# Performance work log

Measured on AMD Instinct MI355X. Metric: run time of the kernel, lower is better.

## Reference

```python
import math
import jax, jax.numpy as jnp
import numpy as np

D_MODEL = 768
N_HEADS = 12
HEAD_DIM = D_MODEL // N_HEADS
D_FF = 3072
LN_EPS = 1e-5


def _alibi_slopes(n_heads):
    def pow2(n):
        start = 2 ** (-(2 ** (-(math.log2(n) - 3))))
        return [start * start ** i for i in range(n)]
    if n_heads & (n_heads - 1) == 0:
        s = pow2(n_heads)
    else:
        c = 2 ** math.floor(math.log2(n_heads))
        s = pow2(c) + pow2(2 * c)[0::2][: n_heads - c]
    return np.asarray(s, dtype=np.float32)  # positive; negated at use site


def _ln(t, g, b):
    m = jnp.mean(t, axis=-1, keepdims=True)
    v = jnp.mean(jnp.square(t - m), axis=-1, keepdims=True)
    return (t - m) * jax.lax.rsqrt(v + LN_EPS) * g + b


def setup_inputs() -> dict:
    key = jax.random.key(0)
    ks = jax.random.split(key, 12)
    B, N = 4, 1025
    s = 0.02
    inp = {
        "x": jax.random.normal(ks[0], (B, N, D_MODEL), dtype=jnp.float32),
        "positions": jax.random.normal(ks[1], (B, N, 2), dtype=jnp.float32) * 8.0,
        "patch_sizes": jax.random.uniform(ks[2], (B,), dtype=jnp.float32, minval=0.5, maxval=2.0),
        "num_registers": 0,
        "ln1_g": jnp.ones((D_MODEL,), jnp.float32),
        "ln1_b": jnp.zeros((D_MODEL,), jnp.float32),
        "wq": jax.random.normal(ks[3], (D_MODEL, D_MODEL), jnp.float32) * s,
        "bq": jnp.zeros((D_MODEL,), jnp.float32),
        "wk": jax.random.normal(ks[4], (D_MODEL, D_MODEL), jnp.float32) * s,
        "bk": jnp.zeros((D_MODEL,), jnp.float32),
        "wv": jax.random.normal(ks[5], (D_MODEL, D_MODEL), jnp.float32) * s,
        "bv": jnp.zeros((D_MODEL,), jnp.float32),
        "wo": jax.random.normal(ks[6], (D_MODEL, D_MODEL), jnp.float32) * s,
        "bo": jnp.zeros((D_MODEL,), jnp.float32),
        "qn_g": jnp.ones((HEAD_DIM,), jnp.float32),
        "qn_b": jnp.zeros((HEAD_DIM,), jnp.float32),
        "kn_g": jnp.ones((HEAD_DIM,), jnp.float32),
        "kn_b": jnp.zeros((HEAD_DIM,), jnp.float32),
        "ln2_g": jnp.ones((D_MODEL,), jnp.float32),
        "ln2_b": jnp.zeros((D_MODEL,), jnp.float32),
        "w1": jax.random.normal(ks[7], (D_MODEL, D_FF), jnp.float32) * s,
        "b1": jnp.zeros((D_FF,), jnp.float32),
        "w2": jax.random.normal(ks[8], (D_FF, D_MODEL), jnp.float32) * s,
        "b2": jnp.zeros((D_MODEL,), jnp.float32),
    }
    return inp


def reference(x, positions, patch_sizes, num_registers,
              ln1_g, ln1_b, wq, bq, wk, bk, wv, bv, wo, bo,
              qn_g, qn_b, kn_g, kn_b, ln2_g, ln2_b, w1, b1, w2, b2):
    B, N, d = x.shape
    H, HD = N_HEADS, HEAD_DIM

    xn = _ln(x, ln1_g, ln1_b)
    q = (xn @ wq + bq).reshape(B, N, H, HD).transpose(0, 2, 1, 3)  # [B,H,N,HD]
    k = (xn @ wk + bk).reshape(B, N, H, HD).transpose(0, 2, 1, 3)
    v = (xn @ wv + bv).reshape(B, N, H, HD).transpose(0, 2, 1, 3)
    q = _ln(q, qn_g, qn_b)  # qk-norm over head_dim
    k = _ln(k, kn_g, kn_b)

    # 2-D ALiBi bias: [B,H,N,N]
    slopes = jnp.asarray(_alibi_slopes(H))  # positive
    ps = jnp.clip(patch_sizes, 1e-6)[:, None, None]
    diff = positions[:, :, None, :] - positions[:, None, :, :]  # [B,N,N,2]
    dist = jnp.sqrt(jnp.sum(jnp.square(diff), axis=-1)) / ps  # [B,N,N]
    bias = -slopes[None, :, None, None] * dist[:, None, :, :]
    idx = jnp.arange(N)
    special = (idx == 0) | ((idx >= 1) & (idx < 1 + num_registers))  # CLS + registers
    keep = (~special).astype(x.dtype)
    bias = bias * keep[None, None, :, None] * keep[None, None, None, :]

    scale = 1.0 / math.sqrt(HD)
    scores = jnp.einsum('bhqd,bhkd->bhqk', q, k) * scale + bias
    attn = jax.nn.softmax(scores, axis=-1)
    o = jnp.einsum('bhqk,bhkd->bhqd', attn, v)
    o = o.transpose(0, 2, 1, 3).reshape(B, N, d) @ wo + bo
    x = x + o

    xn2 = _ln(x, ln2_g, ln2_b)
    mlp = jax.nn.gelu(xn2 @ w1 + b1, approximate=False) @ w2 + b2
    return x + mlp
```

## Files before the change

### kernel.cpp

```cpp
#include <hip/hip_runtime.h>
#include <hip/hip_bf16.h>
#include <math.h>

typedef __attribute__((ext_vector_type(4))) float f32x4;
typedef __attribute__((ext_vector_type(8))) short short8;

#define DMODEL 768
#define NH 12
#define HD 64
#define DFF 3072
#define KVB 64
#define NSPLIT 2
#define QH 2
#define NP 1040

__device__ __forceinline__ short f2bf(float f) {
    union { float f; unsigned int u; } c; c.f = f;
    unsigned int r = c.u + 0x7FFFu + ((c.u >> 16) & 1u);
    return (short)(r >> 16);
}

__device__ __forceinline__ float bf2f(short s) {
    union { unsigned int u; float f; } c; c.u = ((unsigned int)(unsigned short)s) << 16;
    return c.f;
}

__device__ __forceinline__ void gload16(const void* g, void* l) {
    __builtin_amdgcn_global_load_lds((const __attribute__((address_space(1))) void*)g,
                                     (__attribute__((address_space(3))) void*)l, 16, 0, 0);
}

__device__ __forceinline__ int xcd_swz(int o, int nwg) {
    int q = nwg >> 3, r = nwg & 7, x = o & 7, i = o >> 3;
    return (x < r ? x * (q + 1) : r * (q + 1) + (x - r) * q) + i;
}

__global__ __launch_bounds__(256) void transpose_cast(const float* __restrict__ src,
                                                      short* __restrict__ dst, int K, int Nn) {
    __shared__ float tile[32][33];
    const int n0 = blockIdx.x * 32, k0 = blockIdx.y * 32;
    const int tx = threadIdx.x & 31, ty = threadIdx.x >> 5;
    #pragma unroll
    for (int i = ty; i < 32; i += 8) {
        int k = k0 + i, n = n0 + tx;
        tile[i][tx] = (k < K && n < Nn) ? src[(size_t)k * Nn + n] : 0.f;
    }
    __syncthreads();
    #pragma unroll
    for (int i = ty; i < 32; i += 8) {
        int n = n0 + i, k = k0 + tx;
        if (n < Nn && k < K) dst[(size_t)n * K + k] = f2bf(tile[tx][i]);
    }
}

__global__ void concat_bias(const float* __restrict__ bq, const float* __restrict__ bk,
                            const float* __restrict__ bv, float* __restrict__ out) {
    int i = blockIdx.x * 256 + threadIdx.x;
    if (i < 2304) out[i] = (i < 768) ? bq[i] : (i < 1536 ? bk[i - 768] : bv[i - 1536]);
}

__global__ __launch_bounds__(256) void ln_rows(const float* __restrict__ x, const float* __restrict__ g,
                                               const float* __restrict__ bb, short* __restrict__ out, int M) {
    __shared__ float red[8];
    const int row = blockIdx.x;
    const int tid = threadIdx.x;
    const float* xr = x + (size_t)row * DMODEL;
    float v[3];
    #pragma unroll
    for (int j = 0; j < 3; j++) v[j] = xr[tid + j * 256];
    float s = v[0] + v[1] + v[2];
    #pragma unroll
    for (int mk = 32; mk; mk >>= 1) s += __shfl_xor(s, mk);
    if ((tid & 63) == 0) red[tid >> 6] = s;
    __syncthreads();
    const float mean = (red[0] + red[1] + red[2] + red[3]) * (1.0f / 768.0f);
    float sq = 0.f;
    #pragma unroll
    for (int j = 0; j < 3; j++) { float d = v[j] - mean; sq += d * d; }
    #pragma unroll
    for (int mk = 32; mk; mk >>= 1) sq += __shfl_xor(sq, mk);
    if ((tid & 63) == 0) red[4 + (tid >> 6)] = sq;
    __syncthreads();
    const float var = (red[4] + red[5] + red[6] + red[7]) * (1.0f / 768.0f);
    const float rstd = rsqrtf(var + 1e-5f);
    short* orow = out + (size_t)row * DMODEL;
    #pragma unroll
    for (int j = 0; j < 3; j++) {
        int col = tid + j * 256;
        orow[col] = f2bf((v[j] - mean) * rstd * g[col] + bb[col]);
    }
}

__global__ __launch_bounds__(256) void gemm_qkv(const short* __restrict__ A, const short* __restrict__ Bt,
        const float* __restrict__ bias,
        const float* __restrict__ qg, const float* __restrict__ qb2,
        const float* __restrict__ kg, const float* __restrict__ kb2,
        short* __restrict__ Qb, short* __restrict__ Kb, short* __restrict__ Vtp,
        int M, int B, int Nseq) {
    __shared__ short As[64 * 64];
    __shared__ short Bs[128 * 64];
    const int nbx = 18, nby = (M + 63) / 64;
    const int sid = xcd_swz(blockIdx.x, nbx * nby);
    const int n0 = (sid % nbx) * 128, m0 = (sid / nbx) * 64;
    const int tid = threadIdx.x, w = tid >> 6, lane = tid & 63, g = lane >> 4, cl = lane & 15;
    const int wm = w >> 1, wn = w & 1;
    f32x4 acc[2][4];
    #pragma unroll
    for (int a = 0; a < 2; a++)
        #pragma unroll
        for (int b2 = 0; b2 < 4; b2++) acc[a][b2] = (f32x4){0.f, 0.f, 0.f, 0.f};
    for (int kk = 0; kk < 768; kk += 64) {
        #pragma unroll
        for (int c = 0; c < 1536; c += 256) {
            int ci = c + tid;
            if (ci < 512) {
                int row = ci >> 3, p = ci & 7;
                int arow = m0 + row; if (arow >= M) arow = M - 1;
                gload16(A + (size_t)arow * 768 + kk + ((p ^ (row & 7)) << 3), &As[ci * 8]);
            } else {
                int c2 = ci - 512;
                int row = c2 >> 3, p = c2 & 7;
                gload16(Bt + (size_t)(n0 + row) * 768 + kk + ((p ^ (row & 7)) << 3), &Bs[c2 * 8]);
            }
        }
        __syncthreads();
        #pragma unroll
        for (int kh = 0; kh < 2; ++kh) {
            short8 af[2], bf[4];
            #pragma unroll
            for (int mi = 0; mi < 2; mi++) {
                int ra = wm * 32 + mi * 16 + cl;
                af[mi] = *(const short8*)&As[ra * 64 + ((((kh << 2) + g) ^ (ra & 7)) << 3)];
            }
            #pragma unroll
            for (int ni = 0; ni < 4; ni++) {
                int rb = wn * 64 + ni * 16 + cl;
                bf[ni] = *(const short8*)&Bs[rb * 64 + ((((kh << 2) + g) ^ (rb & 7)) << 3)];
            }
            #pragma unroll
            for (int mi = 0; mi < 2; mi++)
                #pragma unroll
                for (int ni = 0; ni < 4; ni++)
                    acc[mi][ni] = __builtin_amdgcn_mfma_f32_16x16x32_bf16(af[mi], bf[ni], acc[mi][ni], 0, 0, 0);
        }
        __syncthreads();
    }
    const int t = n0 / 768;
    const int h = (n0 - t * 768) / 64 + wn;
    const int b0 = m0 / Nseq, bnd = (b0 + 1) * Nseq;
    float bi[4];
    #pragma unroll
    for (int ni = 0; ni < 4; ni++) bi[ni] = bias[n0 + wn * 64 + ni * 16 + cl];
    if (t < 2) {
        const float* gp = (t == 0) ? qg : kg;
        const float* bp = (t == 0) ? qb2 : kb2;
        float gv[4], bv[4];
        #pragma unroll
        for (int ni = 0; ni < 4; ni++) { gv[ni] = gp[ni * 16 + cl]; bv[ni] = bp[ni * 16 + cl]; }
        short* out = (t == 0) ? Qb : Kb;
        #pragma unroll
        for (int mi = 0; mi < 2; mi++)
            #pragma unroll
            for (int r = 0; r < 4; r++) {
                int row = m0 + wm * 32 + mi * 16 + 4 * g + r;
                float v0 = acc[mi][0][r] + bi[0];
                float v1 = acc[mi][1][r] + bi[1];
                float v2 = acc[mi][2][r] + bi[2];
                float v3 = acc[mi][3][r] + bi[3];
                float sx = v0 + v1 + v2 + v3;
                float sxx = v0 * v0 + v1 * v1 + v2 * v2 + v3 * v3;
                #pragma unroll
                for (int mk = 8; mk; mk >>= 1) { sx += __shfl_xor(sx, mk); sxx += __shfl_xor(sxx, mk); }
                float mean = sx * (1.0f / 64.0f);
                float var = sxx * (1.0f / 64.0f) - mean * mean;
                float rstd = rsqrtf(var + 1e-5f);
                if (row < M) {
                    int bb = (row >= bnd) ? b0 + 1 : b0;
                    int n = row - bb * Nseq;
                    size_t base = (((size_t)bb * NH + h) * Nseq + n) * HD + cl;
                    out[base + 0]  = f2bf(fmaf((v0 - mean) * rstd, gv[0], bv[0]));
                    out[base + 16] = f2bf(fmaf((v1 - mean) * rstd, gv[1], bv[1]));
                    out[base + 32] = f2bf(fmaf((v2 - mean) * rstd, gv[2], bv[2]));
                    out[base + 48] = f2bf(fmaf((v3 - mean) * rstd, gv[3], bv[3]));
                }
            }
    } else {
        #pragma unroll
        for (int mi = 0; mi < 2; mi++)
            #pragma unroll
            for (int r = 0; r < 4; r++) {
                int row = m0 + wm * 32 + mi * 16 + 4 * g + r;
                if (row < M) {
                    int bb = (row >= bnd) ? b0 + 1 : b0;
                    int n = row - bb * Nseq;
                    size_t vb2 = ((size_t)bb * NH + h) * HD + cl;
                    #pragma unroll
                    for (int ni = 0; ni < 4; ni++)
                        Vtp[(vb2 + ni * 16) * NP + n] = f2bf(acc[mi][ni][r] + bi[ni]);
                }
            }
    }
}

template<int EPI, int BM, int BN>
__global__ __launch_bounds__(256) void gemm_bt(const short* __restrict__ A, const short* __restrict__ Bt,
        const float* __restrict__ bias, const float* __restrict__ res, void* __restrict__ Cv,
        int M, int Nn, int K) {
    constexpr int RN = BN / 32;
    __shared__ short As[BM * 64];
    __shared__ short Bs[BN * 64];
    const int nbx = Nn / BN, nby = (M + BM - 1) / BM;
    const int sid = xcd_swz(blockIdx.x, nbx * nby);
    const int n0 = (sid % nbx) * BN, m0 = (sid / nbx) * BM;
    const int tid = threadIdx.x, w = tid >> 6, lane = tid & 63, g = lane >> 4, cl = lane & 15;
    const int wm = w >> 1, wn = w & 1;
    f32x4 acc[2][RN];
    #pragma unroll
    for (int a = 0; a < 2; a++)
        #pragma unroll
        for (int b2 = 0; b2 < RN; b2++) acc[a][b2] = (f32x4){0.f, 0.f, 0.f, 0.f};
    constexpr int CHA = BM * 8, CHT = (BM + BN) * 8;
    for (int kk = 0; kk < K; kk += 64) {
        #pragma unroll
        for (int c = 0; c < CHT; c += 256) {
            int ci = c + tid;
            if (ci < CHA) {
                int row = ci >> 3, p = ci & 7;
                int arow = m0 + row; if (arow >= M) arow = M - 1;
                gload16(A + (size_t)arow * K + kk + ((p ^ (row & 7)) << 3), &As[ci * 8]);
            } else {
                int c2 = ci - CHA;
                int row = c2 >> 3, p = c2 & 7;
                gload16(Bt + (size_t)(n0 + row) * K + kk + ((p ^ (row & 7)) << 3), &Bs[c2 * 8]);
            }
        }
        __syncthreads();
        #pragma unroll
        for (int kh = 0; kh < 2; ++kh) {
            short8 af[2], bf[RN];
            #pragma unroll
            for (int mi = 0; mi < 2; mi++) {
                int ra = wm * (BM / 2) + mi * 16 + cl;
                af[mi] = *(const short8*)&As[ra * 64 + ((((kh << 2) + g) ^ (ra & 7)) << 3)];
            }
            #pragma unroll
            for (int ni = 0; ni < RN; ni++) {
                int rb = wn * (BN / 2) + ni * 16 + cl;
                bf[ni] = *(const short8*)&Bs[rb * 64 + ((((kh << 2) + g) ^ (rb & 7)) << 3)];
            }
            #pragma unroll
            for (int mi = 0; mi < 2; mi++)
                #pragma unroll
                for (int ni = 0; ni < RN; ni++)
                    acc[mi][ni] = __builtin_amdgcn_mfma_f32_16x16x32_bf16(af[mi], bf[ni], acc[mi][ni], 0, 0, 0);
        }
        __syncthreads();
    }
    #pragma unroll
    for (int ni = 0; ni < RN; ++ni) {
        int col = n0 + wn * (BN / 2) + ni * 16 + cl;
        float bi = bias[col];
        #pragma unroll
        for (int mi = 0; mi < 2; ++mi) {
            int rb = m0 + wm * (BM / 2) + mi * 16 + 4 * g;
            #pragma unroll
            for (int r = 0; r < 4; ++r) {
                int row = rb + r;
                if (row < M) {
                    float vv = acc[mi][ni][r] + bi;
                    if (EPI == 1) {
                        vv += res[(size_t)row * Nn + col];
                        ((float*)Cv)[(size_t)row * Nn + col] = vv;
                    } else {
                        float ge = 0.5f * vv * (1.0f + erff(vv * 0.70710678118654752f));
                        ((short*)Cv)[(size_t)row * Nn + col] = f2bf(ge);
                    }
                }
            }
        }
    }
}

__global__ __launch_bounds__(256, 2) void attn_kernel(
        const short* __restrict__ Qb, const short* __restrict__ Kb, const short* __restrict__ Vt,
        const float* __restrict__ pos, const float* __restrict__ psz, const int* __restrict__ nregp,
        short* __restrict__ opart, float* __restrict__ ppart, int B, int Nn, int nwg) {
    __shared__ short Vbuf[2][QH][4096];
    __shared__ short Pl[4][QH][16][68];
    const int nqt = (Nn + 63) >> 6;
    const int sid = xcd_swz(blockIdx.x, nwg);
    const int qt = sid % nqt;
    const int rem = sid / nqt;
    const int nyy = (NH / QH) * NSPLIT;
    const int yy = rem % nyy;
    const int b = rem / nyy;
    const int h0 = (yy / NSPLIT) * QH, sp = yy % NSPLIT;
    const int tid = threadIdx.x, w = tid >> 6, lane = tid & 63, g = lane >> 4, cl = lane & 15;
    const int nreg1 = 1 + nregp[0];
    const float inv_ps = 1.0f / fmaxf(psz[b], 1e-6f);
    const float sc2 = 0.125f * 1.4426950408889634f;
    const size_t bq = (size_t)b * Nn;
    const float2* __restrict__ pos2 = (const float2*)pos;
    const int q0 = qt * 64 + w * 16;

    size_t bh[QH], vb[QH];
    float slopeP[QH];
    short8 qa[QH][2];
    int qr = q0 + cl; if (qr > Nn - 1) qr = Nn - 1;
    #pragma unroll
    for (int hh = 0; hh < QH; hh++) {
        int h = h0 + hh;
        bh[hh] = ((size_t)b * NH + h) * (size_t)Nn;
        vb[hh] = ((size_t)b * NH + h) * (size_t)(HD * NP);
        float slope = (h < 8) ? exp2f(-(float)(h + 1)) : exp2f(-0.5f - (float)(h - 8));
        slopeP[hh] = slope * inv_ps * 1.4426950408889634f;
        const short* qptr = Qb + (bh[hh] + qr) * HD;
        qa[hh][0] = *(const short8*)(qptr + 8 * g);
        qa[hh][1] = *(const short8*)(qptr + 32 + 8 * g);
    }

    int qi[4]; float qpx[4], qpy[4], sP[QH][4];
    #pragma unroll
    for (int i = 0; i < 4; i++) {
        qi[i] = q0 + 4 * g + i;
        int qc = qi[i] < Nn ? qi[i] : Nn - 1;
        float2 qp = pos2[bq + qc];
        qpx[i] = qp.x; qpy[i] = qp.y;
        float keepq = (qc < nreg1) ? 0.f : 1.f;
        #pragma unroll
        for (int hh = 0; hh < QH; hh++) sP[hh][i] = slopeP[hh] * keepq;
    }

    f32x4 o[QH][4];
    float psum[QH][4];
    #pragma unroll
    for (int hh = 0; hh < QH; hh++)
        #pragma unroll
        for (int c2 = 0; c2 < 4; c2++) { o[hh][c2] = (f32x4){0.f, 0.f, 0.f, 0.f}; psum[hh][c2] = 0.f; }

    const int ktiles = (Nn + KVB - 1) / KVB;
    const int ktfull = Nn / KVB;
    const int tps = (ktiles + NSPLIT - 1) / NSPLIT;
    const int t0 = sp * tps, t1 = min(ktiles, t0 + tps);

    auto stage = [&](int buf, int kt) {
        const int kv0 = kt * KVB;
        #pragma unroll
        for (int it = 0; it < 2 * QH; ++it) {
            int idx = it * 256 + tid;
            int hh = idx >> 9, rm = idx & 511;
            int d = rm >> 3, slot = rm & 7;
            int kvs = kv0 + ((slot ^ (d & 7)) << 3);
            gload16(Vt + vb[hh] + (size_t)d * NP + kvs, &Vbuf[buf][hh][rm * 8]);
        }
    };

    stage(0, t0);
    int cur = 0;
    for (int kt = t0; kt < t1; ++kt) {
        const int kv0 = kt * KVB;
        __syncthreads();
        if (kt + 1 < t1) stage(cur ^ 1, kt + 1);

        if (kt < ktfull) {
            #pragma unroll
            for (int half = 0; half < 4; ++half) {
                const int kc = kv0 + half * 16 + cl;
                const short* kp0 = Kb + (bh[0] + kc) * HD;
                const short* kp1 = Kb + (bh[1] + kc) * HD;
                const short8 ka0 = *(const short8*)(kp0 + 8 * g);
                const short8 ka1 = *(const short8*)(kp0 + 32 + 8 * g);
                const short8 kb0 = *(const short8*)(kp1 + 8 * g);
                const short8 kb1 = *(const short8*)(kp1 + 32 + 8 * g);
                f32x4 s0 = __builtin_amdgcn_mfma_f32_16x16x32_bf16(qa[0][0], ka0, (f32x4){0.f,0.f,0.f,0.f}, 0, 0, 0);
                s0 = __builtin_amdgcn_mfma_f32_16x16x32_bf16(qa[0][1], ka1, s0, 0, 0, 0);
                f32x4 s1 = __builtin_amdgcn_mfma_f32_16x16x32_bf16(qa[1][0], kb0, (f32x4){0.f,0.f,0.f,0.f}, 0, 0, 0);
                s1 = __builtin_amdgcn_mfma_f32_16x16x32_bf16(qa[1][1], kb1, s1, 0, 0, 0);
                const float2 kp2 = pos2[bq + kc];
                const float kpk = (kc < nreg1) ? 0.f : 1.f;
                #pragma unroll
                for (int i = 0; i < 4; i++) {
                    float dx = qpx[i] - kp2.x, dy = qpy[i] - kp2.y;
                    float dist = sqrtf(fmaf(dx, dx, dy * dy)) * kpk;
                    float e0 = fmaf(s0[i], sc2, -12.0f);
                    e0 = fmaf(-sP[0][i], dist, e0);
                    float p0 = exp2f(e0);
                    unsigned int pu0 = __float_as_uint(p0) & 0xffff0000u;
                    psum[0][i] += __uint_as_float(pu0);
                    Pl[w][0][4 * g + i][half * 16 + cl] = (short)(pu0 >> 16);
                    float e1 = fmaf(s1[i], sc2, -12.0f);
                    e1 = fmaf(-sP[1][i], dist, e1);
                    float p1 = exp2f(e1);
                    unsigned int pu1 = __float_as_uint(p1) & 0xffff0000u;
                    psum[1][i] += __uint_as_float(pu1);
                    Pl[w][1][4 * g + i][half * 16 + cl] = (short)(pu1 >> 16);
                }
            }
        } else {
            #pragma unroll
            for (int half = 0; half < 4; ++half) {
                const int kc = kv0 + half * 16 + cl;
                const int kcc = kc < Nn ? kc : Nn - 1;
                const short* kp0 = Kb + (bh[0] + kcc) * HD;
                const short* kp1 = Kb + (bh[1] + kcc) * HD;
                const short8 ka0 = *(const short8*)(kp0 + 8 * g);
                const short8 ka1 = *(const short8*)(kp0 + 32 + 8 * g);
                const short8 kb0 = *(const short8*)(kp1 + 8 * g);
                const short8 kb1 = *(const short8*)(kp1 + 32 + 8 * g);
                f32x4 s0 = __builtin_amdgcn_mfma_f32_16x16x32_bf16(qa[0][0], ka0, (f32x4){0.f,0.f,0.f,0.f}, 0, 0, 0);
                s0 = __builtin_amdgcn_mfma_f32_16x16x32_bf16(qa[0][1], ka1, s0, 0, 0, 0);
                f32x4 s1 = __builtin_amdgcn_mfma_f32_16x16x32_bf16(qa[1][0], kb0, (f32x4){0.f,0.f,0.f,0.f}, 0, 0, 0);
                s1 = __builtin_amdgcn_mfma_f32_16x16x32_bf16(qa[1][1], kb1, s1, 0, 0, 0);
                const float2 kp2 = pos2[bq + kcc];
                const float kpk = (kcc < nreg1) ? 0.f : 1.f;
                const bool valid = kc < Nn;
                #pragma unroll
                for (int i = 0; i < 4; i++) {
                    float dx = qpx[i] - kp2.x, dy = qpy[i] - kp2.y;
                    float dist = sqrtf(fmaf(dx, dx, dy * dy)) * kpk;
                    float e0 = fmaf(s0[i], sc2, -12.0f);
                    e0 = fmaf(-sP[0][i], dist, e0);
                    float p0 = valid ? exp2f(e0) : 0.f;
                    unsigned int pu0 = __float_as_uint(p0) & 0xffff0000u;
                    psum[0][i] += __uint_as_float(pu0);
                    Pl[w][0][4 * g + i][half * 16 + cl] = (short)(pu0 >> 16);
                    float e1 = fmaf(s1[i], sc2, -12.0f);
                    e1 = fmaf(-sP[1][i], dist, e1);
                    float p1 = valid ? exp2f(e1) : 0.f;
                    unsigned int pu1 = __float_as_uint(p1) & 0xffff0000u;
                    psum[1][i] += __uint_as_float(pu1);
                    Pl[w][1][4 * g + i][half * 16 + cl] = (short)(pu1 >> 16);
                }
            }
        }
        #pragma unroll
        for (int hh = 0; hh < QH; hh++) {
            #pragma unroll
            for (int ks = 0; ks < 2; ++ks) {
                const short8 pf = *(const short8*)&Pl[w][hh][cl][ks * 32 + 8 * g];
                #pragma unroll
                for (int c2 = 0; c2 < 4; c2++) {
                    const int d = c2 * 16 + cl;
                    const int slot = ((ks << 2) + g) ^ (cl & 7);
                    const short8 vf = *(const short8*)&Vbuf[cur][hh][d * 64 + slot * 8];
                    o[hh][c2] = __builtin_amdgcn_mfma_f32_16x16x32_bf16(pf, vf, o[hh][c2], 0, 0, 0);
                }
            }
        }
        cur ^= 1;
    }
    #pragma unroll
    for (int i = 0; i < 4; i++) {
        float rs[QH];
        #pragma unroll
        for (int hh = 0; hh < QH; hh++) {
            rs[hh] = psum[hh][i];
            #pragma unroll
            for (int mk = 8; mk; mk >>= 1) rs[hh] += __shfl_xor(rs[hh], mk);
        }
        if (qi[i] < Nn) {
            #pragma unroll
            for (int hh = 0; hh < QH; hh++) {
                size_t rbase = (((size_t)sp * B + b) * NH + (h0 + hh)) * Nn + qi[i];
                #pragma unroll
                for (int c2 = 0; c2 < 4; c2++)
                    opart[rbase * HD + c2 * 16 + cl] = f2bf(o[hh][c2][i]);
                if (cl == 0) ppart[rbase] = rs[hh];
            }
        }
    }
}

__global__ __launch_bounds__(256) void attn_reduce(const short* __restrict__ opart,
        const float* __restrict__ ppart, short* __restrict__ Ob, int B, int Nn) {
    const int rows = B * NH * Nn;
    const int row = blockIdx.x * 4 + (threadIdx.x >> 6);
    if (row >= rows) return;
    const int d = threadIdx.x & 63;
    const int n = row % Nn;
    const int bh = row / Nn;
    const int h = bh % NH, b = bh / NH;
    const size_t stride = (size_t)B * NH * Nn;
    float o = 0.f, p = 0.f;
    #pragma unroll
    for (int s = 0; s < NSPLIT; s++) {
        o += bf2f(opart[((size_t)s * stride + row) * HD + d]);
        p += ppart[(size_t)s * stride + row];
    }
    Ob[((size_t)b * Nn + n) * DMODEL + h * HD + d] = f2bf(o / p);
}

extern "C" void kernel_launch(void* const* d_in, const int* in_sizes, int n_in,
                              void* d_out, int out_size, void* d_ws, size_t ws_size,
                              hipStream_t stream) {
    const float* x    = (const float*)d_in[0];
    const float* pos  = (const float*)d_in[1];
    const float* psz  = (const float*)d_in[2];
    const int*   nreg = (const int*)d_in[3];
    const float* ln1g = (const float*)d_in[4];
    const float* ln1b = (const float*)d_in[5];
    const float* wq   = (const float*)d_in[6];
    const float* bq   = (const float*)d_in[7];
    const float* wk   = (const float*)d_in[8];
    const float* bk   = (const float*)d_in[9];
    const float* wv   = (const float*)d_in[10];
    const float* bv   = (const float*)d_in[11];
    const float* wo   = (const float*)d_in[12];
    const float* bo   = (const float*)d_in[13];
    const float* qng  = (const float*)d_in[14];
    const float* qnb  = (const float*)d_in[15];
    const float* kng  = (const float*)d_in[16];
    const float* knb  = (const float*)d_in[17];
    const float* ln2g = (const float*)d_in[18];
    const float* ln2b = (const float*)d_in[19];
    const float* w1   = (const float*)d_in[20];
    const float* b1   = (const float*)d_in[21];
    const float* w2   = (const float*)d_in[22];
    const float* b2   = (const float*)d_in[23];

    const int B  = in_sizes[2];
    const int Nn = in_sizes[1] / (2 * B);
    const int M  = B * Nn;

    char* ws = (char*)d_ws;
    size_t off = 0;
    auto alloc = [&](size_t bytes) -> char* {
        char* p = ws + off;
        off += (bytes + 255) & ~(size_t)255;
        return p;
    };
    short* wt_qkv   = (short*)alloc((size_t)2304 * 768 * 2);
    short* wt_o     = (short*)alloc((size_t)768 * 768 * 2);
    short* wt_1     = (short*)alloc((size_t)3072 * 768 * 2);
    short* wt_2     = (short*)alloc((size_t)768 * 3072 * 2);
    float* bias_qkv = (float*)alloc(2304 * 4);
    short* xn       = (short*)alloc((size_t)M * 768 * 2);
    short* Qb       = (short*)alloc((size_t)M * 768 * 2);
    short* Kb       = (short*)alloc((size_t)M * 768 * 2);
    short* Vt       = (short*)alloc((size_t)B * NH * HD * NP * 2 + 4096);
    short* Ob       = (short*)alloc((size_t)M * 768 * 2);
    float* x1       = (float*)alloc((size_t)M * 768 * 4);
    short* xn2      = (short*)alloc((size_t)M * 768 * 2);
    short* hmid     = (short*)alloc((size_t)M * 3072 * 2);
    float* ppart    = (float*)alloc((size_t)NSPLIT * B * NH * Nn * 4);
    short* opart    = hmid;

    dim3 blk(256);
    transpose_cast<<<dim3(24, 24), blk, 0, stream>>>(wq, wt_qkv, 768, 768);
    transpose_cast<<<dim3(24, 24), blk, 0, stream>>>(wk, wt_qkv + 768 * 768, 768, 768);
    transpose_cast<<<dim3(24, 24), blk, 0, stream>>>(wv, wt_qkv + 2 * 768 * 768, 768, 768);
    transpose_cast<<<dim3(24, 24), blk, 0, stream>>>(wo, wt_o, 768, 768);
    transpose_cast<<<dim3(96, 24), blk, 0, stream>>>(w1, wt_1, 768, 3072);
    transpose_cast<<<dim3(24, 96), blk, 0, stream>>>(w2, wt_2, 3072, 768);
    concat_bias<<<9, blk, 0, stream>>>(bq, bk, bv, bias_qkv);

    const int MB64 = (M + 63) / 64;
    ln_rows<<<M, blk, 0, stream>>>(x, ln1g, ln1b, xn, M);
    gemm_qkv<<<18 * MB64, blk, 0, stream>>>(xn, wt_qkv, bias_qkv, qng, qnb, kng, knb,
                                            Qb, Kb, Vt, M, B, Nn);
    const int nqt = (Nn + 63) / 64;
    const int anwg = nqt * (NH / QH) * NSPLIT * B;
    attn_kernel<<<anwg, blk, 0, stream>>>(Qb, Kb, Vt, pos, psz, nreg, opart, ppart, B, Nn, anwg);
    attn_reduce<<<(B * NH * Nn + 3) / 4, blk, 0, stream>>>(opart, ppart, Ob, B, Nn);
    gemm_bt<1, 64, 64><<<12 * MB64, blk, 0, stream>>>(Ob, wt_o, bo, x, x1, M, 768, 768);
    ln_rows<<<M, blk, 0, stream>>>(x1, ln2g, ln2b, xn2, M);
    gemm_bt<2, 64, 128><<<24 * MB64, blk, 0, stream>>>(xn2, wt_1, b1, nullptr, hmid, M, 3072, 768);
    gemm_bt<1, 64, 64><<<12 * MB64, blk, 0, stream>>>(hmid, wt_2, b2, x1, (float*)d_out, M, 768, 3072);
}
```

Baseline: 270.1 us.

## Transpose QK MFMA so each lane owns one query, pack P to bf16, split KV three ways

Swaps the MFMA operand order so each lane holds scores for a single query row across four keys. Per-query position, slope and keep factors then collapse to scalars, and per-iteration mask work is only specialised in for tiles touching the CLS/register tokens. P values are converted with packed bf16 conversion and written as 32-bit words into a padded LDS tile. Row sums are reduced with fewer shuffles plus an LDS exchange. KV is split three ways with launch bounds raised to three blocks per CU, which may raise register pressure and adds partial-result reduction work. The row sums now accumulate unrounded fp32 p rather than the bf16-truncated values used in PV.

```diff
diff --git a/kernel.cpp b/kernel.cpp
--- a/kernel.cpp
+++ b/kernel.cpp
@@ -10,9 +10,12 @@
 #define HD 64
 #define DFF 3072
 #define KVB 64
-#define NSPLIT 2
+#define NSPLIT 3
 #define QH 2
 #define NP 1040
+
+struct FalseC { static constexpr bool v = false; };
+struct TrueC  { static constexpr bool v = true;  };
 
 __device__ __forceinline__ short f2bf(float f) {
     union { float f; unsigned int u; } c; c.f = f;
@@ -281,12 +284,13 @@
     }
 }
 
-__global__ __launch_bounds__(256, 2) void attn_kernel(
+__global__ __launch_bounds__(256, 3) void attn_kernel(
         const short* __restrict__ Qb, const short* __restrict__ Kb, const short* __restrict__ Vt,
         const float* __restrict__ pos, const float* __restrict__ psz, const int* __restrict__ nregp,
         short* __restrict__ opart, float* __restrict__ ppart, int B, int Nn, int nwg) {
     __shared__ short Vbuf[2][QH][4096];
-    __shared__ short Pl[4][QH][16][68];
+    __shared__ short Pl[4][QH][16][72];
+    __shared__ float Rs[4][QH][16];
     const int nqt = (Nn + 63) >> 6;
     const int sid = xcd_swz(blockIdx.x, nwg);
     const int qt = sid % nqt;
@@ -304,42 +308,35 @@
     const int q0 = qt * 64 + w * 16;
 
     size_t bh[QH], vb[QH];
-    float slopeP[QH];
     short8 qa[QH][2];
+    float sP[QH];
     int qr = q0 + cl; if (qr > Nn - 1) qr = Nn - 1;
+    const float2 qp = pos2[bq + qr];
+    const float keepq = (qr < nreg1) ? 0.f : 1.f;
     #pragma unroll
     for (int hh = 0; hh < QH; hh++) {
         int h = h0 + hh;
         bh[hh] = ((size_t)b * NH + h) * (size_t)Nn;
         vb[hh] = ((size_t)b * NH + h) * (size_t)(HD * NP);
         float slope = (h < 8) ? exp2f(-(float)(h + 1)) : exp2f(-0.5f - (float)(h - 8));
-        slopeP[hh] = slope * inv_ps * 1.4426950408889634f;
+        sP[hh] = slope * inv_ps * 1.4426950408889634f * keepq;
         const short* qptr = Qb + (bh[hh] + qr) * HD;
         qa[hh][0] = *(const short8*)(qptr + 8 * g);
         qa[hh][1] = *(const short8*)(qptr + 32 + 8 * g);
     }
 
-    int qi[4]; float qpx[4], qpy[4], sP[QH][4];
-    #pragma unroll
-    for (int i = 0; i < 4; i++) {
-        qi[i] = q0 + 4 * g + i;
-        int qc = qi[i] < Nn ? qi[i] : Nn - 1;
-        float2 qp = pos2[bq + qc];
-        qpx[i] = qp.x; qpy[i] = qp.y;
-        float keepq = (qc < nreg1) ? 0.f : 1.f;
-        #pragma unroll
-        for (int hh = 0; hh < QH; hh++) sP[hh][i] = slopeP[hh] * keepq;
-    }
+    int qi[4];
+    #pragma unroll
+    for (int i = 0; i < 4; i++) qi[i] = q0 + 4 * g + i;
 
     f32x4 o[QH][4];
-    float psum[QH][4];
+    float psum[QH] = {0.f, 0.f};
     #pragma unroll
     for (int hh = 0; hh < QH; hh++)
         #pragma unroll
-        for (int c2 = 0; c2 < 4; c2++) { o[hh][c2] = (f32x4){0.f, 0.f, 0.f, 0.f}; psum[hh][c2] = 0.f; }
+        for (int c2 = 0; c2 < 4; c2++) o[hh][c2] = (f32x4){0.f, 0.f, 0.f, 0.f};
 
     const int ktiles = (Nn + KVB - 1) / KVB;
-    const int ktfull = Nn / KVB;
     const int tps = (ktiles + NSPLIT - 1) / NSPLIT;
     const int t0 = sp * tps, t1 = min(ktiles, t0 + tps);
 
@@ -362,77 +359,67 @@
         __syncthreads();
         if (kt + 1 < t1) stage(cur ^ 1, kt + 1);
 
-        if (kt < ktfull) {
-            #pragma unroll
-            for (int half = 0; half < 4; ++half) {
-                const int kc = kv0 + half * 16 + cl;
-                const short* kp0 = Kb + (bh[0] + kc) * HD;
-                const short* kp1 = Kb + (bh[1] + kc) * HD;
-                const short8 ka0 = *(const short8*)(kp0 + 8 * g);
-                const short8 ka1 = *(const short8*)(kp0 + 32 + 8 * g);
-                const short8 kb0 = *(const short8*)(kp1 + 8 * g);
-                const short8 kb1 = *(const short8*)(kp1 + 32 + 8 * g);
-                f32x4 s0 = __builtin_amdgcn_mfma_f32_16x16x32_bf16(qa[0][0], ka0, (f32x4){0.f,0.f,0.f,0.f}, 0, 0, 0);
-                s0 = __builtin_amdgcn_mfma_f32_16x16x32_bf16(qa[0][1], ka1, s0, 0, 0, 0);
-                f32x4 s1 = __builtin_amdgcn_mfma_f32_16x16x32_bf16(qa[1][0], kb0, (f32x4){0.f,0.f,0.f,0.f}, 0, 0, 0);
-                s1 = __builtin_amdgcn_mfma_f32_16x16x32_bf16(qa[1][1], kb1, s1, 0, 0, 0);
-                const float2 kp2 = pos2[bq + kc];
-                const float kpk = (kc < nreg1) ? 0.f : 1.f;
-                #pragma unroll
-                for (int i = 0; i < 4; i++) {
-                    float dx = qpx[i] - kp2.x, dy = qpy[i] - kp2.y;
-                    float dist = sqrtf(fmaf(dx, dx, dy * dy)) * kpk;
-                    float e0 = fmaf(s0[i], sc2, -12.0f);
-                    e0 = fmaf(-sP[0][i], dist, e0);
-                    float p0 = exp2f(e0);
-                    unsigned int pu0 = __float_as_uint(p0) & 0xffff0000u;
-                    psum[0][i] += __uint_as_float(pu0);
-                    Pl[w][0][4 * g + i][half * 16 + cl] = (short)(pu0 >> 16);
-                    float e1 = fmaf(s1[i], sc2, -12.0f);
-                    e1 = fmaf(-sP[1][i], dist, e1);
-                    float p1 = exp2f(e1);
-                    unsigned int pu1 = __float_as_uint(p1) & 0xffff0000u;
-                    psum[1][i] += __uint_as_float(pu1);
-                    Pl[w][1][4 * g + i][half * 16 + cl] = (short)(pu1 >> 16);
-                }
+        auto qbody = [&](int qt2, auto mc, auto tc) {
+            constexpr bool KMASK = decltype(mc)::v;
+            constexpr bool TAIL  = decltype(tc)::v;
+            const int kbase = kv0 + qt2 * 16;
+            int krow = kbase + cl;
+            if (TAIL) krow = min(krow, Nn - 1);
+            const short* kp0 = Kb + (bh[0] + krow) * HD;
+            const short* kp1 = Kb + (bh[1] + krow) * HD;
+            const short8 k00 = *(const short8*)(kp0 + 8 * g);
+            const short8 k01 = *(const short8*)(kp0 + 32 + 8 * g);
+            const short8 k10 = *(const short8*)(kp1 + 8 * g);
+            const short8 k11 = *(const short8*)(kp1 + 32 + 8 * g);
+            f32x4 s0 = __builtin_amdgcn_mfma_f32_16x16x32_bf16(k00, qa[0][0], (f32x4){0.f,0.f,0.f,0.f}, 0, 0, 0);
+            s0 = __builtin_amdgcn_mfma_f32_16x16x32_bf16(k01, qa[0][1], s0, 0, 0, 0);
+            f32x4 s1 = __builtin_amdgcn_mfma_f32_16x16x32_bf16(k10, qa[1][0], (f32x4){0.f,0.f,0.f,0.f}, 0, 0, 0);
+            s1 = __builtin_amdgcn_mfma_f32_16x16x32_bf16(k11, qa[1][1], s1, 0, 0, 0);
+            const int kb4 = kbase + 4 * g;
+            float p0v[4], p1v[4];
+            #pragma unroll
+            for (int i = 0; i < 4; i++) {
+                int ki = kb4 + i;
+                int kic = TAIL ? min(ki, Nn - 1) : ki;
+                float2 kp2 = pos2[bq + kic];
+                float dx = qp.x - kp2.x, dy = qp.y - kp2.y;
+                float dist = sqrtf(fmaf(dx, dx, dy * dy));
+                if (KMASK) dist *= (ki < nreg1) ? 0.f : 1.f;
+                float e0 = fmaf(s0[i], sc2, -12.0f);
+                e0 = fmaf(-sP[0], dist, e0);
+                float p0 = exp2f(e0);
+                float e1 = fmaf(s1[i], sc2, -12.0f);
+                e1 = fmaf(-sP[1], dist, e1);
+                float p1 = exp2f(e1);
+                if (TAIL) { bool vl = ki < Nn; p0 = vl ? p0 : 0.f; p1 = vl ? p1 : 0.f; }
+                psum[0] += p0; psum[1] += p1;
+                p0v[i] = p0; p1v[i] = p1;
+            }
+            unsigned int w00, w01, w10, w11;
+            asm("v_cvt_pk_bf16_f32 %0, %1, %2" : "=v"(w00) : "v"(p0v[0]), "v"(p0v[1]));
+            asm("v_cvt_pk_bf16_f32 %0, %1, %2" : "=v"(w01) : "v"(p0v[2]), "v"(p0v[3]));
+            asm("v_cvt_pk_bf16_f32 %0, %1, %2" : "=v"(w10) : "v"(p1v[0]), "v"(p1v[1]));
+            asm("v_cvt_pk_bf16_f32 %0, %1, %2" : "=v"(w11) : "v"(p1v[2]), "v"(p1v[3]));
+            *(unsigned int*)&Pl[w][0][cl][qt2 * 16 + 4 * g]     = w00;
+            *(unsigned int*)&Pl[w][0][cl][qt2 * 16 + 4 * g + 2] = w01;
+            *(unsigned int*)&Pl[w][1][cl][qt2 * 16 + 4 * g]     = w10;
+            *(unsigned int*)&Pl[w][1][cl][qt2 * 16 + 4 * g + 2] = w11;
+        };
+
+        const bool istail = (kv0 + KVB > Nn);
+        if (!istail) {
+            if (kv0 < nreg1) {
+                qbody(0, TrueC{}, FalseC{}); qbody(1, TrueC{}, FalseC{});
+                qbody(2, TrueC{}, FalseC{}); qbody(3, TrueC{}, FalseC{});
+            } else {
+                qbody(0, FalseC{}, FalseC{}); qbody(1, FalseC{}, FalseC{});
+                qbody(2, FalseC{}, FalseC{}); qbody(3, FalseC{}, FalseC{});
             }
         } else {
-            #pragma unroll
-            for (int half = 0; half < 4; ++half) {
-                const int kc = kv0 + half * 16 + cl;
-                const int kcc = kc < Nn ? kc : Nn - 1;
-                const short* kp0 = Kb + (bh[0] + kcc) * HD;
-                const short* kp1 = Kb + (bh[1] + kcc) * HD;
-                const short8 ka0 = *(const short8*)(kp0 + 8 * g);
-                const short8 ka1 = *(const short8*)(kp0 + 32 + 8 * g);
-                const short8 kb0 = *(const short8*)(kp1 + 8 * g);
-                const short8 kb1 = *(const short8*)(kp1 + 32 + 8 * g);
-                f32x4 s0 = __builtin_amdgcn_mfma_f32_16x16x32_bf16(qa[0][0], ka0, (f32x4){0.f,0.f,0.f,0.f}, 0, 0, 0);
-                s0 = __builtin_amdgcn_mfma_f32_16x16x32_bf16(qa[0][1], ka1, s0, 0, 0, 0);
-                f32x4 s1 = __builtin_amdgcn_mfma_f32_16x16x32_bf16(qa[1][0], kb0, (f32x4){0.f,0.f,0.f,0.f}, 0, 0, 0);
-                s1 = __builtin_amdgcn_mfma_f32_16x16x32_bf16(qa[1][1], kb1, s1, 0, 0, 0);
-                const float2 kp2 = pos2[bq + kcc];
-                const float kpk = (kcc < nreg1) ? 0.f : 1.f;
-                const bool valid = kc < Nn;
-                #pragma unroll
-                for (int i = 0; i < 4; i++) {
-                    float dx = qpx[i] - kp2.x, dy = qpy[i] - kp2.y;
-                    float dist = sqrtf(fmaf(dx, dx, dy * dy)) * kpk;
-                    float e0 = fmaf(s0[i], sc2, -12.0f);
-                    e0 = fmaf(-sP[0][i], dist, e0);
-                    float p0 = valid ? exp2f(e0) : 0.f;
-                    unsigned int pu0 = __float_as_uint(p0) & 0xffff0000u;
-                    psum[0][i] += __uint_as_float(pu0);
-                    Pl[w][0][4 * g + i][half * 16 + cl] = (short)(pu0 >> 16);
-                    float e1 = fmaf(s1[i], sc2, -12.0f);
-                    e1 = fmaf(-sP[1][i], dist, e1);
-                    float p1 = valid ? exp2f(e1) : 0.f;
-                    unsigned int pu1 = __float_as_uint(p1) & 0xffff0000u;
-                    psum[1][i] += __uint_as_float(pu1);
-                    Pl[w][1][4 * g + i][half * 16 + cl] = (short)(pu1 >> 16);
-                }
-            }
-        }
+            qbody(0, FalseC{}, TrueC{}); qbody(1, FalseC{}, TrueC{});
+            qbody(2, FalseC{}, TrueC{}); qbody(3, FalseC{}, TrueC{});
+        }
+
         #pragma unroll
         for (int hh = 0; hh < QH; hh++) {
             #pragma unroll
@@ -449,15 +436,18 @@
         }
         cur ^= 1;
     }
+
+    #pragma unroll
+    for (int hh = 0; hh < QH; hh++) {
+        float r = psum[hh];
+        r += __shfl_xor(r, 16);
+        r += __shfl_xor(r, 32);
+        if (lane < 16) Rs[w][hh][lane] = r;
+    }
+    float4 rs0 = *(const float4*)&Rs[w][0][4 * g];
+    float4 rs1 = *(const float4*)&Rs[w][1][4 * g];
     #pragma unroll
     for (int i = 0; i < 4; i++) {
-        float rs[QH];
-        #pragma unroll
-        for (int hh = 0; hh < QH; hh++) {
-            rs[hh] = psum[hh][i];
-            #pragma unroll
-            for (int mk = 8; mk; mk >>= 1) rs[hh] += __shfl_xor(rs[hh], mk);
-        }
         if (qi[i] < Nn) {
             #pragma unroll
             for (int hh = 0; hh < QH; hh++) {
@@ -465,7 +455,7 @@
                 #pragma unroll
                 for (int c2 = 0; c2 < 4; c2++)
                     opart[rbase * HD + c2 * 16 + cl] = f2bf(o[hh][c2][i]);
-                if (cl == 0) ppart[rbase] = rs[hh];
+                if (cl == 0) ppart[rbase] = hh ? rs1[i] : rs0[i];
             }
         }
     }
```

After: 264.7 us. -2.0%, faster.
